# Performance work log

Measured on AMD Instinct MI355X. Metric: run time of the kernel, lower is better.

## Reference

```python
import jax, jax.numpy as jnp
import numpy as np

GENE_DIM = 3008   # conf.gene_dim
H = 6             # conf.num_hiddens_genotype (per-term hidden dim)
D_MODEL = 768     # conf.d_model
B = 4096          # batch
SIZES = [2048, 512, 128, 32, 8, 1]   # terms per topological layer (leaves -> root)
GPL = 8           # direct genes per leaf term
EPS = 1e-5        # BatchNorm1d eps


def setup_inputs() -> dict:
    key = jax.random.key(0)
    keys = iter(jax.random.split(key, 64))

    def rn(shape, scale=0.05):
        return jax.random.normal(next(keys), shape, dtype=jnp.float32) * scale

    inp = {"x": jax.random.normal(next(keys), (B, GENE_DIM), dtype=jnp.float32)}
    # batched per-leaf direct_gene_layer: Linear(GENE_DIM, GPL) for each leaf term
    inp["Wg"] = rn((SIZES[0], GPL, GENE_DIM))
    inp["bg"] = rn((SIZES[0], GPL))
    # per-layer term linear + batchnorm params; input sizes per layer
    in_sizes = [GPL, 4 * H, 4 * H, 4 * H, 4 * H, 8 * H]
    for i, (t, c) in enumerate(zip(SIZES, in_sizes)):
        inp[f"W{i}"] = rn((t, H, c))
        inp[f"b{i}"] = rn((t, H))
        inp[f"gm{i}"] = jnp.ones((t, H), jnp.float32)
        inp[f"bt{i}"] = jnp.zeros((t, H), jnp.float32)
    inp["Wf"] = rn((D_MODEL, H))
    inp["bf"] = rn((D_MODEL,))
    return inp


def _term_layer(child, W, b, gm, bt):
    # child: [B, T, in] ; W: [T, H, in] -> per-term Linear + tanh + BatchNorm1d(train)
    h = jnp.tanh(jnp.einsum('bti,toi->bto', child, W) + b)
    mu = h.mean(axis=0)              # [T, H] batch stats (biased var, as torch BN)
    var = h.var(axis=0)
    return (h - mu) * jax.lax.rsqrt(var + EPS) * gm + bt


def reference(x, Wg, bg,
              W0, b0, gm0, bt0, W1, b1, gm1, bt1, W2, b2, gm2, bt2,
              W3, b3, gm3, bt3, W4, b4, gm4, bt4, W5, b5, gm5, bt5,
              Wf, bf):
    gene = x[:, :GENE_DIM].astype(jnp.float32)        # x.narrow(1, 0, gene_dim)
    # all leaf direct_gene_layers batched: [B, T0, GPL]
    g = jnp.einsum('bg,tog->bto', gene, Wg) + bg
    h = _term_layer(g, W0, b0, gm0, bt0)              # leaf term layer: [B, T0, H]
    layer_params = [(W1, b1, gm1, bt1), (W2, b2, gm2, bt2), (W3, b3, gm3, bt3),
                    (W4, b4, gm4, bt4), (W5, b5, gm5, bt5)]
    for (W, b, gm, bt), T in zip(layer_params, SIZES[1:]):
        # gather-concat of child term outputs: contiguous fanout blocks -> reshape
        child = h.reshape(h.shape[0], T, -1)          # [B, T, fanout*H]
        h = _term_layer(child, W, b, gm, bt)
    root = h[:, 0, :]                                 # [B, H]
    return root @ Wf.T + bf                           # final_linear_layer -> [B, D_MODEL]
```

## Files before the change

### kernel.cpp

```cpp
#include <hip/hip_runtime.h>


typedef float f32x4 __attribute__((ext_vector_type(4)));
typedef __bf16 bf16x8 __attribute__((ext_vector_type(8)));

#define GL2LDS(g, l)                                                          \
  __builtin_amdgcn_global_load_lds(                                           \
      (__attribute__((address_space(1))) void*)(g),                           \
      (__attribute__((address_space(3))) void*)(l), 16, 0, 0)

__device__ __forceinline__ unsigned short f2bf(float f) {
  unsigned int u = __float_as_uint(f);
  u = u + 0x7fffu + ((u >> 16) & 1u);
  return (unsigned short)(u >> 16);
}

__device__ __forceinline__ float bf2f(unsigned int lo16) {
  return __uint_as_float(lo16 << 16);
}

__device__ __forceinline__ float tanh_fast(float x) {
  float e = __expf(2.0f * x);
  return 1.0f - __fdividef(2.0f, e + 1.0f);
}

__global__ __launch_bounds__(256) void cvt_f32_bf16(
    const float* __restrict__ in, unsigned short* __restrict__ out, int n4) {
  int i = blockIdx.x * 256 + threadIdx.x;
  if (i < n4) {
    float4 v = ((const float4*)in)[i];
    ushort4 o;
    o.x = f2bf(v.x); o.y = f2bf(v.y); o.z = f2bf(v.z); o.w = f2bf(v.w);
    ((ushort4*)out)[i] = o;
  }
}

__global__ __launch_bounds__(256, 2) void gemm_fused(
    const unsigned short* __restrict__ A, const unsigned short* __restrict__ Bm,
    const float* __restrict__ bg, const float* __restrict__ W0,
    const float* __restrict__ b0, unsigned short* __restrict__ h0,
    float* __restrict__ stats) {
  constexpr int N = 16384, K = 3008, WOUT = 12288;
  __shared__ unsigned short smem[128 * 128];
  __shared__ float sW0[16 * 6 * 8];
  __shared__ float sb0[16 * 6];
  unsigned short* As = smem;
  unsigned short* Bs = smem + 128 * 64;

  const int tid = threadIdx.x;
  const int w = tid >> 6, l = tid & 63;

  const int lin = blockIdx.x;
  const int xc = lin & 7, q = lin >> 3;
  const int mt = xc * 4 + (q & 3), nt = q >> 2;
  const int m0 = mt * 128, n0 = nt * 128;
  const int tB = nt * 16;

  for (int i = tid; i < 768; i += 256) sW0[i] = W0[(size_t)tB * 48 + i];
  if (tid < 96) sb0[tid] = b0[tB * 6 + tid];

  const int srow = tid >> 3;
  const int cs = (tid & 7) ^ (srow & 7);
  const unsigned short* gA = A + (size_t)(m0 + srow) * K + cs * 8;
  const unsigned short* gB = Bm + (size_t)(n0 + srow) * K + cs * 8;
  unsigned short* lA = As + w * 512;
  unsigned short* lB = Bs + w * 512;

  f32x4 acc[4][4];
#pragma unroll
  for (int i = 0; i < 4; ++i)
#pragma unroll
    for (int j = 0; j < 4; ++j) acc[i][j] = (f32x4)0.0f;

  const int quad = l >> 4;
  const int lrow = l & 15;
  const int wm = (w >> 1) * 64, wn = (w & 1) * 64;

  for (int k0 = 0; k0 < K; k0 += 64) {
#pragma unroll
    for (int j = 0; j < 4; ++j) {
      GL2LDS(gA + (size_t)j * 32 * K + k0, lA + j * 2048);
      GL2LDS(gB + (size_t)j * 32 * K + k0, lB + j * 2048);
    }
    __syncthreads();
#pragma unroll
    for (int kk = 0; kk < 2; ++kk) {
      bf16x8 av[4], bv[4];
#pragma unroll
      for (int f = 0; f < 4; ++f) {
        int ra = wm + f * 16 + lrow;
        int ca = (kk * 4 + quad) ^ (ra & 7);
        av[f] = *(const bf16x8*)(As + ra * 64 + ca * 8);
        int rb = wn + f * 16 + lrow;
        int cb = (kk * 4 + quad) ^ (rb & 7);
        bv[f] = *(const bf16x8*)(Bs + rb * 64 + cb * 8);
      }
#pragma unroll
      for (int fm = 0; fm < 4; ++fm)
#pragma unroll
        for (int fn = 0; fn < 4; ++fn)
          acc[fm][fn] = __builtin_amdgcn_mfma_f32_16x16x32_bf16(
              av[fm], bv[fn], acc[fm][fn], 0, 0, 0);
    }
    __syncthreads();
  }

  float bgv[4];
#pragma unroll
  for (int fn = 0; fn < 4; ++fn) bgv[fn] = bg[n0 + wn + fn * 16 + lrow];
#pragma unroll
  for (int fm = 0; fm < 4; ++fm) {
#pragma unroll
    for (int fn = 0; fn < 4; ++fn) {
      int nloc = wn + fn * 16 + lrow;
      int c = nloc >> 3, ci = nloc & 7;
#pragma unroll
      for (int r = 0; r < 4; ++r) {
        int m = wm + fm * 16 + quad * 4 + r;
        int off = (((m >> 2) & 3) << 1) | (m & 1);
        smem[m * 128 + ((c ^ off) << 3) + ci] =
            f2bf(acc[fm][fn][r] + bgv[fn]);
      }
    }
  }
  __syncthreads();

  const int t = tid >> 4;
  const int mgrp = tid & 15;
  const int tg = tB + t;
  float ls[6], lq[6];
#pragma unroll
  for (int o = 0; o < 6; ++o) { ls[o] = 0.0f; lq[o] = 0.0f; }

#pragma unroll
  for (int rr = 0; rr < 8; ++rr) {
    int m = mgrp * 8 + rr;
    int off = (((m >> 2) & 3) << 1) | (m & 1);
    uint4 u = *(const uint4*)(smem + m * 128 + ((t ^ off) << 3));
    float ch[8];
    ch[0] = bf2f(u.x & 0xffffu); ch[1] = bf2f(u.x >> 16);
    ch[2] = bf2f(u.y & 0xffffu); ch[3] = bf2f(u.y >> 16);
    ch[4] = bf2f(u.z & 0xffffu); ch[5] = bf2f(u.z >> 16);
    ch[6] = bf2f(u.w & 0xffffu); ch[7] = bf2f(u.w >> 16);
    unsigned int pk[3];
    unsigned short hb[6];
#pragma unroll
    for (int o = 0; o < 6; ++o) {
      float a = sb0[t * 6 + o];
      const float* wr = &sW0[(t * 6 + o) * 8];
#pragma unroll
      for (int j = 0; j < 8; ++j) a += ch[j] * wr[j];
      float h = tanh_fast(a);
      ls[o] += h; lq[o] += h * h;
      hb[o] = f2bf(h);
    }
    pk[0] = (unsigned int)hb[0] | ((unsigned int)hb[1] << 16);
    pk[1] = (unsigned int)hb[2] | ((unsigned int)hb[3] << 16);
    pk[2] = (unsigned int)hb[4] | ((unsigned int)hb[5] << 16);
    unsigned int* op = (unsigned int*)(h0 + (size_t)(m0 + m) * WOUT + tg * 6);
    op[0] = pk[0]; op[1] = pk[1]; op[2] = pk[2];
  }

#pragma unroll
  for (int o = 0; o < 6; ++o) {
#pragma unroll
    for (int d = 8; d > 0; d >>= 1) {
      ls[o] += __shfl_xor(ls[o], d, 16);
      lq[o] += __shfl_xor(lq[o], d, 16);
    }
  }
  if (mgrp == 0) {
#pragma unroll
    for (int o = 0; o < 6; ++o) {
      atomicAdd(&stats[tg * 6 + o], ls[o]);
      atomicAdd(&stats[WOUT + tg * 6 + o], lq[o]);
    }
  }
}

template <int NCOL>
__device__ __forceinline__ void load_row(const unsigned short* p, float* d) {
  static_assert(NCOL % 8 == 0, "");
#pragma unroll
  for (int i = 0; i < NCOL / 8; ++i) {
    uint4 u = *(const uint4*)(p + i * 8);
    d[i * 8 + 0] = bf2f(u.x & 0xffffu); d[i * 8 + 1] = bf2f(u.x >> 16);
    d[i * 8 + 2] = bf2f(u.y & 0xffffu); d[i * 8 + 3] = bf2f(u.y >> 16);
    d[i * 8 + 4] = bf2f(u.z & 0xffffu); d[i * 8 + 5] = bf2f(u.z >> 16);
    d[i * 8 + 6] = bf2f(u.w & 0xffffu); d[i * 8 + 7] = bf2f(u.w >> 16);
  }
}
template <int NCOL>
__device__ __forceinline__ void load_row(const float* p, float* d) {
  static_assert(NCOL % 4 == 0, "");
#pragma unroll
  for (int i = 0; i < NCOL / 4; ++i) {
    float4 v = *(const float4*)(p + i * 4);
    d[i * 4 + 0] = v.x; d[i * 4 + 1] = v.y;
    d[i * 4 + 2] = v.z; d[i * 4 + 3] = v.w;
  }
}

template <typename TIN, typename TOUT, int T, int IC>
__global__ __launch_bounds__(256) void term_layer(
    const TIN* __restrict__ in, const float* __restrict__ prevStats,
    const float* __restrict__ prevGm, const float* __restrict__ prevBt,
    const float* __restrict__ W, const float* __restrict__ bvec,
    TOUT* __restrict__ out, float* __restrict__ curStats) {
  constexpr int WIN = T * IC;
  constexpr int WOUT = T * 6;
  const int tB = blockIdx.x;

  __shared__ float sW[6 * IC];
  __shared__ float sB[6];
  __shared__ float sScale[IC];
  __shared__ float sShift[IC];
  for (int i = threadIdx.x; i < 6 * IC; i += 256)
    sW[i] = W[(size_t)tB * 6 * IC + i];
  if (threadIdx.x < 6) sB[threadIdx.x] = bvec[tB * 6 + threadIdx.x];
  if (threadIdx.x < IC) {
    int c = threadIdx.x;
    int gc = tB * IC + c;
    float mu = prevStats[gc] * (1.0f / 4096.0f);
    float var = prevStats[WIN + gc] * (1.0f / 4096.0f) - mu * mu;
    float sc = rsqrtf(var + 1e-5f) * prevGm[gc];
    sScale[c] = sc;
    sShift[c] = prevBt[gc] - mu * sc;
  }
  __syncthreads();

  float ls[6], lq[6];
#pragma unroll
  for (int i = 0; i < 6; ++i) { ls[i] = 0.0f; lq[i] = 0.0f; }

  const int bchunk = 4096 / gridDim.y;
  const int b0 = blockIdx.y * bchunk;
  for (int b = b0 + (int)threadIdx.x; b < b0 + bchunk; b += 256) {
    float child[IC];
    load_row<IC>(in + (size_t)b * WIN + (size_t)tB * IC, child);
#pragma unroll
    for (int c = 0; c < IC; ++c)
      child[c] = child[c] * sScale[c] + sShift[c];
    float hv[6];
#pragma unroll
    for (int o = 0; o < 6; ++o) {
      float a = sB[o];
      const float* wr = &sW[o * IC];
#pragma unroll
      for (int j = 0; j < IC; ++j) a += child[j] * wr[j];
      float h = tanh_fast(a);
      hv[o] = h;
      ls[o] += h;
      lq[o] += h * h;
    }
    TOUT* op = out + (size_t)b * WOUT + tB * 6;
    if constexpr (sizeof(TOUT) == 2) {
      unsigned int* oi = (unsigned int*)op;
#pragma unroll
      for (int i = 0; i < 3; ++i)
        oi[i] = (unsigned int)f2bf(hv[2 * i]) |
                ((unsigned int)f2bf(hv[2 * i + 1]) << 16);
    } else {
#pragma unroll
      for (int i = 0; i < 6; ++i) op[i] = hv[i];
    }
  }

#pragma unroll
  for (int i = 0; i < 6; ++i) {
    float s = ls[i], qq = lq[i];
#pragma unroll
    for (int d = 32; d > 0; d >>= 1) {
      s += __shfl_down(s, d, 64);
      qq += __shfl_down(qq, d, 64);
    }
    if ((threadIdx.x & 63) == 0) {
      atomicAdd(&curStats[tB * 6 + i], s);
      atomicAdd(&curStats[WOUT + tB * 6 + i], qq);
    }
  }
}

__global__ __launch_bounds__(256) void final_fc(
    const float* __restrict__ h5, const float* __restrict__ stats5,
    const float* __restrict__ gm5, const float* __restrict__ bt5,
    const float* __restrict__ Wf, const float* __restrict__ bfv,
    float* __restrict__ out) {
  __shared__ float sWf[768 * 6];
  __shared__ float sbf[768];
  __shared__ float sRoot[8][6];
  const int tid = threadIdx.x;
  for (int i = tid; i < 768 * 6; i += 256) sWf[i] = Wf[i];
  for (int i = tid; i < 768; i += 256) sbf[i] = bfv[i];
  const int b0 = blockIdx.x * 8;
  if (tid < 48) {
    int bb = tid / 6, o = tid % 6;
    float mu = stats5[o] * (1.0f / 4096.0f);
    float var = stats5[6 + o] * (1.0f / 4096.0f) - mu * mu;
    float sc = rsqrtf(var + 1e-5f) * gm5[o];
    sRoot[bb][o] = (h5[(size_t)(b0 + bb) * 6 + o] - mu) * sc + bt5[o];
  }
  __syncthreads();
#pragma unroll
  for (int bb = 0; bb < 8; ++bb) {
    float r0 = sRoot[bb][0], r1 = sRoot[bb][1], r2 = sRoot[bb][2];
    float r3 = sRoot[bb][3], r4 = sRoot[bb][4], r5 = sRoot[bb][5];
    for (int d = tid; d < 768; d += 256) {
      const float* wr = &sWf[d * 6];
      float a = sbf[d] + r0 * wr[0] + r1 * wr[1] + r2 * wr[2] +
                r3 * wr[3] + r4 * wr[4] + r5 * wr[5];
      out[(size_t)(b0 + bb) * 768 + d] = a;
    }
  }
}

extern "C" void kernel_launch(void* const* d_in, const int* in_sizes, int n_in,
                              void* d_out, int out_size, void* d_ws,
                              size_t ws_size, hipStream_t stream) {
  const float* x   = (const float*)d_in[0];
  const float* Wg  = (const float*)d_in[1];
  const float* bg  = (const float*)d_in[2];
  const float* W0  = (const float*)d_in[3];
  const float* b0v = (const float*)d_in[4];
  const float* gm0 = (const float*)d_in[5];
  const float* bt0 = (const float*)d_in[6];
  const float* W1  = (const float*)d_in[7];
  const float* b1v = (const float*)d_in[8];
  const float* gm1 = (const float*)d_in[9];
  const float* bt1 = (const float*)d_in[10];
  const float* W2  = (const float*)d_in[11];
  const float* b2v = (const float*)d_in[12];
  const float* gm2 = (const float*)d_in[13];
  const float* bt2 = (const float*)d_in[14];
  const float* W3  = (const float*)d_in[15];
  const float* b3v = (const float*)d_in[16];
  const float* gm3 = (const float*)d_in[17];
  const float* bt3 = (const float*)d_in[18];
  const float* W4  = (const float*)d_in[19];
  const float* b4v = (const float*)d_in[20];
  const float* gm4 = (const float*)d_in[21];
  const float* bt4 = (const float*)d_in[22];
  const float* W5  = (const float*)d_in[23];
  const float* b5v = (const float*)d_in[24];
  const float* gm5 = (const float*)d_in[25];
  const float* bt5 = (const float*)d_in[26];
  const float* Wf  = (const float*)d_in[27];
  const float* bfv = (const float*)d_in[28];

  char* ws = (char*)d_ws;
  unsigned short* Xb  = (unsigned short*)(ws + 0);
  unsigned short* Wgb = (unsigned short*)(ws + 24641536ULL);
  unsigned short* h0  = (unsigned short*)(ws + 123207680ULL);
  unsigned short* h1  = (unsigned short*)(ws + 223870976ULL);
  unsigned short* h2  = (unsigned short*)(ws + 249036800ULL);
  float* h3 = (float*)(ws + 255328256ULL);
  float* h4 = (float*)(ws + 258473984ULL);
  float* h5 = (float*)(ws + 259260416ULL);
  float* stats = (float*)(ws + 259358720ULL);

  hipMemsetAsync(stats, 0, 131072, stream);

  cvt_f32_bf16<<<dim3(12032), 256, 0, stream>>>(x, Xb, 12320768 / 4);
  cvt_f32_bf16<<<dim3(48128), 256, 0, stream>>>(Wg, Wgb, 49283072 / 4);

  gemm_fused<<<dim3(4096), 256, 0, stream>>>(Xb, Wgb, bg, W0, b0v, h0,
                                             stats + 0);

  term_layer<unsigned short, unsigned short, 512, 24>
      <<<dim3(512, 4), 256, 0, stream>>>(h0, stats + 0, gm0, bt0, W1, b1v, h1,
                                         stats + 24576);
  term_layer<unsigned short, unsigned short, 128, 24>
      <<<dim3(128, 16), 256, 0, stream>>>(h1, stats + 24576, gm1, bt1, W2, b2v,
                                          h2, stats + 30720);
  term_layer<unsigned short, float, 32, 24>
      <<<dim3(32, 16), 256, 0, stream>>>(h2, stats + 30720, gm2, bt2, W3, b3v,
                                         h3, stats + 32256);
  term_layer<float, float, 8, 24>
      <<<dim3(8, 16), 256, 0, stream>>>(h3, stats + 32256, gm3, bt3, W4, b4v,
                                        h4, stats + 32640);
  term_layer<float, float, 1, 48>
      <<<dim3(1, 16), 256, 0, stream>>>(h4, stats + 32640, gm4, bt4, W5, b5v,
                                        h5, stats + 32736);

  final_fc<<<dim3(512), 256, 0, stream>>>(h5, stats + 32736, gm5, bt5, Wf, bfv,
                                          (float*)d_out);
}
```

Baseline: 1.034 ms.

## Halve GEMM epilogue LDS footprint, merge conversion kernels, widen term-layer grid

```diff
diff --git a/kernel.cpp b/kernel.cpp
--- a/kernel.cpp
+++ b/kernel.cpp
@@ -24,15 +24,26 @@
   return 1.0f - __fdividef(2.0f, e + 1.0f);
 }
 
-__global__ __launch_bounds__(256) void cvt_f32_bf16(
-    const float* __restrict__ in, unsigned short* __restrict__ out, int n4) {
+__global__ __launch_bounds__(256) void cvt_all(
+    const float* __restrict__ x, const float* __restrict__ wg,
+    unsigned short* __restrict__ xb, unsigned short* __restrict__ wgb) {
+  constexpr int NX = 12320768 / 4;
+  constexpr int NW = 49283072 / 4;
   int i = blockIdx.x * 256 + threadIdx.x;
-  if (i < n4) {
-    float4 v = ((const float4*)in)[i];
-    ushort4 o;
-    o.x = f2bf(v.x); o.y = f2bf(v.y); o.z = f2bf(v.z); o.w = f2bf(v.w);
-    ((ushort4*)out)[i] = o;
-  }
+  const float* src;
+  unsigned short* dst;
+  int j;
+  if (i < NX) {
+    src = x; dst = xb; j = i;
+  } else {
+    j = i - NX;
+    if (j >= NW) return;
+    src = wg; dst = wgb;
+  }
+  float4 v = ((const float4*)src)[j];
+  ushort4 o;
+  o.x = f2bf(v.x); o.y = f2bf(v.y); o.z = f2bf(v.z); o.w = f2bf(v.w);
+  ((ushort4*)dst)[j] = o;
 }
 
 __global__ __launch_bounds__(256, 2) void gemm_fused(
@@ -41,9 +52,7 @@
     const float* __restrict__ b0, unsigned short* __restrict__ h0,
     float* __restrict__ stats) {
   constexpr int N = 16384, K = 3008, WOUT = 12288;
-  __shared__ unsigned short smem[128 * 128];
-  __shared__ float sW0[16 * 6 * 8];
-  __shared__ float sb0[16 * 6];
+  __shared__ unsigned short smem[128 * 64 * 2];
   unsigned short* As = smem;
   unsigned short* Bs = smem + 128 * 64;
 
@@ -55,9 +64,6 @@
   const int mt = xc * 4 + (q & 3), nt = q >> 2;
   const int m0 = mt * 128, n0 = nt * 128;
   const int tB = nt * 16;
-
-  for (int i = tid; i < 768; i += 256) sW0[i] = W0[(size_t)tB * 48 + i];
-  if (tid < 96) sb0[tid] = b0[tB * 6 + tid];
 
   const int srow = tid >> 3;
   const int cs = (tid & 7) ^ (srow & 7);
@@ -105,25 +111,16 @@
     __syncthreads();
   }
 
+  float* sW0 = (float*)smem;
+  float* sb0 = ((float*)smem) + 768;
+  unsigned short* Cs = Bs;
+
+  for (int i = tid; i < 768; i += 256) sW0[i] = W0[(size_t)tB * 48 + i];
+  if (tid < 96) sb0[tid] = b0[tB * 6 + tid];
+
   float bgv[4];
 #pragma unroll
   for (int fn = 0; fn < 4; ++fn) bgv[fn] = bg[n0 + wn + fn * 16 + lrow];
-#pragma unroll
-  for (int fm = 0; fm < 4; ++fm) {
-#pragma unroll
-    for (int fn = 0; fn < 4; ++fn) {
-      int nloc = wn + fn * 16 + lrow;
-      int c = nloc >> 3, ci = nloc & 7;
-#pragma unroll
-      for (int r = 0; r < 4; ++r) {
-        int m = wm + fm * 16 + quad * 4 + r;
-        int off = (((m >> 2) & 3) << 1) | (m & 1);
-        smem[m * 128 + ((c ^ off) << 3) + ci] =
-            f2bf(acc[fm][fn][r] + bgv[fn]);
-      }
-    }
-  }
-  __syncthreads();
 
   const int t = tid >> 4;
   const int mgrp = tid & 15;
@@ -133,32 +130,55 @@
   for (int o = 0; o < 6; ++o) { ls[o] = 0.0f; lq[o] = 0.0f; }
 
 #pragma unroll
-  for (int rr = 0; rr < 8; ++rr) {
-    int m = mgrp * 8 + rr;
-    int off = (((m >> 2) & 3) << 1) | (m & 1);
-    uint4 u = *(const uint4*)(smem + m * 128 + ((t ^ off) << 3));
-    float ch[8];
-    ch[0] = bf2f(u.x & 0xffffu); ch[1] = bf2f(u.x >> 16);
-    ch[2] = bf2f(u.y & 0xffffu); ch[3] = bf2f(u.y >> 16);
-    ch[4] = bf2f(u.z & 0xffffu); ch[5] = bf2f(u.z >> 16);
-    ch[6] = bf2f(u.w & 0xffffu); ch[7] = bf2f(u.w >> 16);
-    unsigned int pk[3];
-    unsigned short hb[6];
-#pragma unroll
-    for (int o = 0; o < 6; ++o) {
-      float a = sb0[t * 6 + o];
-      const float* wr = &sW0[(t * 6 + o) * 8];
-#pragma unroll
-      for (int j = 0; j < 8; ++j) a += ch[j] * wr[j];
-      float h = tanh_fast(a);
-      ls[o] += h; lq[o] += h * h;
-      hb[o] = f2bf(h);
-    }
-    pk[0] = (unsigned int)hb[0] | ((unsigned int)hb[1] << 16);
-    pk[1] = (unsigned int)hb[2] | ((unsigned int)hb[3] << 16);
-    pk[2] = (unsigned int)hb[4] | ((unsigned int)hb[5] << 16);
-    unsigned int* op = (unsigned int*)(h0 + (size_t)(m0 + m) * WOUT + tg * 6);
-    op[0] = pk[0]; op[1] = pk[1]; op[2] = pk[2];
+  for (int half = 0; half < 2; ++half) {
+    if ((w >> 1) == half) {
+#pragma unroll
+      for (int fm = 0; fm < 4; ++fm) {
+#pragma unroll
+        for (int fn = 0; fn < 4; ++fn) {
+          int n = wn + fn * 16 + lrow;
+          int c = n >> 3, ci = n & 7;
+#pragma unroll
+          for (int r = 0; r < 4; ++r) {
+            int mloc = fm * 16 + quad * 4 + r;
+            int off = (((mloc >> 2) & 3) << 1) | (mloc & 1);
+            Cs[mloc * 128 + (((c ^ off)) << 3) + ci] =
+                f2bf(acc[fm][fn][r] + bgv[fn]);
+          }
+        }
+      }
+    }
+    __syncthreads();
+
+#pragma unroll
+    for (int rr = 0; rr < 4; ++rr) {
+      int mloc = mgrp * 4 + rr;
+      int m = half * 64 + mloc;
+      int off = (((mloc >> 2) & 3) << 1) | (mloc & 1);
+      uint4 u = *(const uint4*)(Cs + mloc * 128 + ((t ^ off) << 3));
+      float ch[8];
+      ch[0] = bf2f(u.x & 0xffffu); ch[1] = bf2f(u.x >> 16);
+      ch[2] = bf2f(u.y & 0xffffu); ch[3] = bf2f(u.y >> 16);
+      ch[4] = bf2f(u.z & 0xffffu); ch[5] = bf2f(u.z >> 16);
+      ch[6] = bf2f(u.w & 0xffffu); ch[7] = bf2f(u.w >> 16);
+      unsigned short hb[6];
+#pragma unroll
+      for (int o = 0; o < 6; ++o) {
+        float a = sb0[t * 6 + o];
+        const float* wr = &sW0[(t * 6 + o) * 8];
+#pragma unroll
+        for (int j = 0; j < 8; ++j) a += ch[j] * wr[j];
+        float h = tanh_fast(a);
+        ls[o] += h; lq[o] += h * h;
+        hb[o] = f2bf(h);
+      }
+      unsigned int* op =
+          (unsigned int*)(h0 + (size_t)(m0 + m) * WOUT + tg * 6);
+      op[0] = (unsigned int)hb[0] | ((unsigned int)hb[1] << 16);
+      op[1] = (unsigned int)hb[2] | ((unsigned int)hb[3] << 16);
+      op[2] = (unsigned int)hb[4] | ((unsigned int)hb[5] << 16);
+    }
+    __syncthreads();
   }
 
 #pragma unroll
@@ -360,14 +380,13 @@
 
   hipMemsetAsync(stats, 0, 131072, stream);
 
-  cvt_f32_bf16<<<dim3(12032), 256, 0, stream>>>(x, Xb, 12320768 / 4);
-  cvt_f32_bf16<<<dim3(48128), 256, 0, stream>>>(Wg, Wgb, 49283072 / 4);
+  cvt_all<<<dim3(60160), 256, 0, stream>>>(x, Wg, Xb, Wgb);
 
   gemm_fused<<<dim3(4096), 256, 0, stream>>>(Xb, Wgb, bg, W0, b0v, h0,
                                              stats + 0);
 
   term_layer<unsigned short, unsigned short, 512, 24>
-      <<<dim3(512, 4), 256, 0, stream>>>(h0, stats + 0, gm0, bt0, W1, b1v, h1,
+      <<<dim3(512, 8), 256, 0, stream>>>(h0, stats + 0, gm0, bt0, W1, b1v, h1,
                                          stats + 24576);
   term_layer<unsigned short, unsigned short, 128, 24>
       <<<dim3(128, 16), 256, 0, stream>>>(h1, stats + 24576, gm1, bt1, W2, b2v,
```

Measured after the change: 1.151 ms. 11.3% more time.
